# Optimization experiments

Hardware: AMD Instinct MI355X
Metric: run time of the kernel (lower is better)

The kernel has to match this reference:

```python
import jax, jax.numpy as jnp
import numpy as np

B, C, H, W = 8, 128, 64, 64
K = 3
MID = C // 4  # reduction=4


def setup_inputs() -> dict:
    key = jax.random.key(0)
    ks = jax.random.split(key, 8)
    f = lambda k, s, sc=1.0: jax.random.normal(k, s, dtype=jnp.float32) * sc
    return {
        "X2": f(ks[0], (B, C, H, W)),
        "Y2": f(ks[1], (B, C, H, W)),
        "static_w": f(ks[2], (C, 1, K, K), 0.1),        # depthwise conv weight (OIHW, groups=C)
        "w1": f(ks[3], (2 * MID, 2 * C), 0.05),          # context_conv1 1x1
        "w2": f(ks[4], (2 * MID, 2 * MID), 0.05),        # context_conv2 1x1
        "w3": f(ks[5], (C * K * K, 2 * MID), 0.05),      # context_conv3 1x1
        "ws": f(ks[6], (K * K, 2 * C), 0.05),            # spatial_conv 1x1
        "wf": f(ks[7], (C, 2 * C), 0.05),                # fusion_conv 1x1
    }


def _c1x1(w, x):
    # 1x1 conv, no bias: (O,I) x (B,I,H,W) -> (B,O,H,W)
    return jnp.einsum('oc,bchw->bohw', w, x)


def reference(X2, Y2, static_w, w1, w2, w3, ws, wf):
    Bn, Cn, Hn, Wn = X2.shape
    Kn = static_w.shape[-1]
    pad = (Kn - 1) // 2

    # static depthwise conv
    Xs = jax.lax.conv_general_dilated(
        X2, static_w, window_strides=(1, 1), padding='SAME',
        feature_group_count=Cn, dimension_numbers=('NCHW', 'OIHW', 'NCHW'))

    Fc = jnp.concatenate([Xs, Y2], axis=1)  # (B, 2C, H, W)

    # SE-style context branch: 1x1 conv -> global avg pool -> 1x1 -> relu -> 1x1
    ctx = _c1x1(w1, Fc).mean(axis=(2, 3))                  # (B, 2*mid)
    ctx = jax.nn.relu(jnp.einsum('oc,bc->bo', w2, ctx))    # (B, 2*mid)
    channel_filter = jnp.einsum('oc,bc->bo', w3, ctx)      # (B, C*k*k)
    channel_filter = channel_filter.reshape(Bn, Cn, Kn * Kn, 1, 1)

    spatial_filter = _c1x1(ws, Fc).reshape(Bn, 1, Kn * Kn, Hn, Wn)
    dynamic_filter = channel_filter + spatial_filter       # (B, C, k*k, H, W)

    # unfold X2: patch order matches F.unfold (channel-major, kernel row-major)
    Xp = jnp.pad(X2, ((0, 0), (0, 0), (pad, pad), (pad, pad)))
    patches = jnp.stack(
        [Xp[:, :, i:i + Hn, j:j + Wn] for i in range(Kn) for j in range(Kn)],
        axis=2)                                            # (B, C, k*k, H, W)

    dynamic_out = (patches * dynamic_filter).sum(axis=2)   # (B, C, H, W)

    out = _c1x1(wf, jnp.concatenate([Xs, dynamic_out], axis=1))
    return out
```

## Files before the change

kernel.cpp:

```cpp
#include <hip/hip_runtime.h>
#include <hip/hip_bf16.h>

#define Bn 8
#define Cn 128
#define Hn 64
#define Wn 64
#define HWn 4096
#define KK 9

typedef short short8 __attribute__((ext_vector_type(8)));
typedef float f32x4 __attribute__((ext_vector_type(4)));

__device__ inline unsigned short f2b(float v) {
    __hip_bfloat16 h = __float2bfloat16(v);
    return *reinterpret_cast<unsigned short*>(&h);
}

__global__ __launch_bounds__(256) void k_pre(
    const float* __restrict__ X2, const float* __restrict__ Y2,
    float* __restrict__ pws)
{
    int bc = blockIdx.x, t = threadIdx.x;
    const float4* xp = (const float4*)(X2 + (size_t)bc * HWn);
    const float4* yp = (const float4*)(Y2 + (size_t)bc * HWn);
    float v[10];
#pragma unroll
    for (int k = 0; k < 10; k++) v[k] = 0.f;
#pragma unroll
    for (int i = 0; i < 4; i++) {
        int q = t + i * 256;
        float4 x = xp[q], y = yp[q];
        float s4 = x.x + x.y + x.z + x.w;
        v[0] += s4;
        v[5] += y.x + y.y + y.z + y.w;
        int px = q * 4, h = px >> 6, w4 = px & 63;
        if (h == 0)   v[1] += s4;
        if (h == 63)  v[2] += s4;
        if (w4 == 0)  v[3] += x.x;
        if (w4 == 60) v[4] += x.w;
        if (px == 0)    v[6] += x.x;
        if (px == 60)   v[7] += x.w;
        if (px == 4032) v[8] += x.x;
        if (px == 4092) v[9] += x.w;
    }
#pragma unroll
    for (int k = 0; k < 10; k++)
#pragma unroll
        for (int off = 32; off; off >>= 1)
            v[k] += __shfl_down(v[k], off);
    __shared__ float red[4][10];
    int lane = t & 63, wv = t >> 6;
    if (lane == 0) {
#pragma unroll
        for (int k = 0; k < 10; k++) red[wv][k] = v[k];
    }
    __syncthreads();
    if (t < 10) pws[bc * 10 + t] = red[0][t] + red[1][t] + red[2][t] + red[3][t];
}

__global__ __launch_bounds__(256) void k_ctx(
    const float* __restrict__ pws, const float* __restrict__ sw,
    const float* __restrict__ w1, const float* __restrict__ w2,
    const float* __restrict__ w3, const float* __restrict__ wf,
    const float* __restrict__ wsp, float* __restrict__ cf,
    unsigned short* __restrict__ wfb, unsigned short* __restrict__ wsb)
{
    int blk = blockIdx.x, b = blk >> 2, qd = blk & 3;
    int t = threadIdx.x;
    for (int i = t; i < 1024; i += 256) {
        int j = blk * 1024 + i;
        wfb[j] = f2b(wf[j]);
    }
    {
        int j = blk * 128 + t;
        if (t < 128) {
            int tt = j >> 8, c = j & 255;
            wsb[j] = (tt < KK) ? f2b(wsp[tt * 256 + c]) : (unsigned short)0;
        }
    }
    __shared__ float mfc[256], c1[64], c2[64];
    if (t < 128) {
        const float* S = pws + (b * Cn + t) * 10;
        float T = S[0];
        float R[3]  = { S[2], 0.f, S[1] };
        float Cc[3] = { S[4], 0.f, S[3] };
        float Xc[3][3] = {{S[9], 0.f, S[8]}, {0.f, 0.f, 0.f}, {S[7], 0.f, S[6]}};
        float a = 0.f;
#pragma unroll
        for (int i = 0; i < 3; i++)
#pragma unroll
            for (int j = 0; j < 3; j++)
                a += sw[t * 9 + i * 3 + j] * (T - R[i] - Cc[j] + Xc[i][j]);
        mfc[t] = a * (1.f / HWn);
    } else {
        mfc[t] = pws[(b * Cn + (t - 128)) * 10 + 5] * (1.f / HWn);
    }
    __syncthreads();
    if (t < 64) {
        const float4* wr = (const float4*)(w1 + t * 256);
        float a = 0.f;
        for (int c = 0; c < 64; c++) {
            float4 v = wr[c];
            a += v.x * mfc[c*4] + v.y * mfc[c*4+1] + v.z * mfc[c*4+2] + v.w * mfc[c*4+3];
        }
        c1[t] = a;
    }
    __syncthreads();
    if (t < 64) {
        const float4* wr = (const float4*)(w2 + t * 64);
        float a = 0.f;
        for (int c = 0; c < 16; c++) {
            float4 v = wr[c];
            a += v.x * c1[c*4] + v.y * c1[c*4+1] + v.z * c1[c*4+2] + v.w * c1[c*4+3];
        }
        c2[t] = fmaxf(a, 0.f);
    }
    __syncthreads();
    for (int j = qd * 288 + t; j < qd * 288 + 288; j += 256) {
        const float4* wr = (const float4*)(w3 + j * 64);
        float a = 0.f;
        for (int c = 0; c < 16; c++) {
            float4 v = wr[c];
            a += v.x * c2[c*4] + v.y * c2[c*4+1] + v.z * c2[c*4+2] + v.w * c2[c*4+3];
        }
        cf[b * Cn * KK + j] = a;
    }
}

__global__ __launch_bounds__(512, 4) void k_main(
    const float* __restrict__ X2, const float* __restrict__ Y2,
    const float* __restrict__ sw,
    const unsigned short* __restrict__ wfb, const unsigned short* __restrict__ wsb,
    const float* __restrict__ cf, float* __restrict__ out)
{
    __shared__ unsigned short sFt[2][Wn][Cn];
    __shared__ float sSf[KK][Wn];
    __shared__ float sCfP[Cn][12];
    __shared__ float sSwP[Cn][12];

    int bid = blockIdx.x;
    int b = bid & 7, h = bid >> 3;
    int t = threadIdx.x;
    int w = t & 63, cg = t >> 6;
    int swz = (w & 7) << 3;
    int c0 = cg * 16;

    for (int i = t; i < Cn * KK; i += 512) {
        int c = i / 9, q = i - c * 9;
        sSwP[c][q] = sw[i];
        sCfP[c][q] = cf[b * Cn * KK + i];
    }
    __syncthreads();

    const float* xcol = X2 + (size_t)(b * Cn + c0) * HWn + h * Wn + w;
    const float* ycol = Y2 + (size_t)(b * Cn + c0) * HWn + h * Wn + w;
    bool hm = h > 0, hp = h < Hn - 1;
    bool wm = w > 0, wp = w < Wn - 1;

    float tap[16][3];

    {
        unsigned int px[4], py[4];
#pragma unroll
        for (int i = 0; i < 16; i++) {
            int c = c0 + i;
            const float* xp = xcol + (size_t)i * HWn;
            float r0 = hm ? xp[-Wn] : 0.f;
            float r1 = xp[0];
            float r2 = hp ? xp[Wn] : 0.f;
            tap[i][0] = r0; tap[i][1] = r1; tap[i][2] = r2;
            float4 k0 = *(const float4*)&sSwP[c][0];
            float4 k1 = *(const float4*)&sSwP[c][4];
            float  k8 = sSwP[c][8];
            float xl0 = __shfl_up(r0, 1), xr0 = __shfl_down(r0, 1);
            float xl1 = __shfl_up(r1, 1), xr1 = __shfl_down(r1, 1);
            float xl2 = __shfl_up(r2, 1), xr2 = __shfl_down(r2, 1);
            if (!wm) { xl0 = 0.f; xl1 = 0.f; xl2 = 0.f; }
            if (!wp) { xr0 = 0.f; xr1 = 0.f; xr2 = 0.f; }
            float a = k0.x * xl0 + k0.y * r0 + k0.z * xr0
                    + k0.w * xl1 + k1.x * r1 + k1.y * xr1
                    + k1.z * xl2 + k1.w * r2 + k8 * xr2;
            float yv = ycol[(size_t)i * HWn];
            unsigned int ah = f2b(a), yh = f2b(yv);
            int sub = i & 7;
            if ((sub & 1) == 0) { px[sub >> 1] = ah; py[sub >> 1] = yh; }
            else { px[sub >> 1] |= ah << 16; py[sub >> 1] |= yh << 16; }
            if (sub == 7) {
                int col = (c - 7) ^ swz;
                *(uint4*)(&sFt[0][w][col]) = *(uint4*)px;
                *(uint4*)(&sFt[1][w][col]) = *(uint4*)py;
            }
        }
    }
    __syncthreads();

    {
        int lane = t & 63, wv = t >> 6;
        int l16 = lane & 15, half = lane >> 4, kk = half * 8;
        if (wv < 4) {
            int wA = wv * 16 + l16;
            int swzA = (wA & 7) << 3;
            f32x4 acc = (f32x4){0.f, 0.f, 0.f, 0.f};
#pragma unroll
            for (int ks = 0; ks < 8; ks++) {
                short8 av = *(const short8*)(wsb + l16 * 256 + ks * 32 + kk);
                int col = (((ks & 3) * 32 + kk)) ^ swzA;
                short8 bv = *(const short8*)(&sFt[ks >> 2][wA][0] + col);
                acc = __builtin_amdgcn_mfma_f32_16x16x32_bf16(av, bv, acc, 0, 0, 0);
            }
#pragma unroll
            for (int r = 0; r < 4; r++) {
                int tt = half * 4 + r;
                if (tt < KK) sSf[tt][wA] = acc[r];
            }
        }
    }
    __syncthreads();

    {
        float sfw[9];
#pragma unroll
        for (int q = 0; q < 9; q++) sfw[q] = sSf[q][w];
        unsigned int pd[4];
#pragma unroll
        for (int i = 0; i < 16; i++) {
            int c = c0 + i;
            float r0 = tap[i][0], r1 = tap[i][1], r2 = tap[i][2];
            float4 e0 = *(const float4*)&sCfP[c][0];
            float4 e1 = *(const float4*)&sCfP[c][4];
            float  e8 = sCfP[c][8];
            float xl0 = __shfl_up(r0, 1), xr0 = __shfl_down(r0, 1);
            float xl1 = __shfl_up(r1, 1), xr1 = __shfl_down(r1, 1);
            float xl2 = __shfl_up(r2, 1), xr2 = __shfl_down(r2, 1);
            if (!wm) { xl0 = 0.f; xl1 = 0.f; xl2 = 0.f; }
            if (!wp) { xr0 = 0.f; xr1 = 0.f; xr2 = 0.f; }
            float a = (e0.x + sfw[0]) * xl0 + (e0.y + sfw[1]) * r0 + (e0.z + sfw[2]) * xr0
                    + (e0.w + sfw[3]) * xl1 + (e1.x + sfw[4]) * r1 + (e1.y + sfw[5]) * xr1
                    + (e1.z + sfw[6]) * xl2 + (e1.w + sfw[7]) * r2 + (e8 + sfw[8]) * xr2;
            unsigned int ah = f2b(a);
            int sub = i & 7;
            if ((sub & 1) == 0) pd[sub >> 1] = ah;
            else pd[sub >> 1] |= ah << 16;
            if (sub == 7) {
                int col = (c - 7) ^ swz;
                *(uint4*)(&sFt[1][w][col]) = *(uint4*)pd;
            }
        }
    }
    __syncthreads();

    {
        int lane = t & 63, wv = t >> 6;
        int l16 = lane & 15, half = lane >> 4, kk = half * 8;
        int o0 = wv * 16;
        f32x4 acc[4];
#pragma unroll
        for (int n = 0; n < 4; n++) acc[n] = (f32x4){0.f, 0.f, 0.f, 0.f};
#pragma unroll
        for (int ks = 0; ks < 8; ks++) {
            int bufi = ks >> 2;
            int kc = (ks & 3) * 32 + kk;
            short8 av = *(const short8*)(wfb + (o0 + l16) * 256 + ks * 32 + kk);
#pragma unroll
            for (int n = 0; n < 4; n++) {
                int wB = n * 16 + l16;
                int col = kc ^ ((wB & 7) << 3);
                short8 bv = *(const short8*)(&sFt[bufi][wB][0] + col);
                acc[n] = __builtin_amdgcn_mfma_f32_16x16x32_bf16(av, bv, acc[n], 0, 0, 0);
            }
        }
        size_t obase = (size_t)b * Cn * HWn + (size_t)h * Wn;
#pragma unroll
        for (int n = 0; n < 4; n++)
#pragma unroll
            for (int r = 0; r < 4; r++) {
                int o = o0 + half * 4 + r;
                out[obase + (size_t)o * HWn + n * 16 + l16] = acc[n][r];
            }
    }
}

extern "C" void kernel_launch(void* const* d_in, const int* in_sizes, int n_in,
                              void* d_out, int out_size, void* d_ws, size_t ws_size,
                              hipStream_t stream) {
    (void)in_sizes; (void)n_in; (void)out_size; (void)ws_size;
    const float* X2  = (const float*)d_in[0];
    const float* Y2  = (const float*)d_in[1];
    const float* sw  = (const float*)d_in[2];
    const float* w1  = (const float*)d_in[3];
    const float* w2  = (const float*)d_in[4];
    const float* w3  = (const float*)d_in[5];
    const float* wsp = (const float*)d_in[6];
    const float* wf  = (const float*)d_in[7];
    float* out = (float*)d_out;

    float* wsf = (float*)d_ws;
    float* pws = wsf;
    float* cf  = wsf + 10240;
    unsigned short* wfb = (unsigned short*)(wsf + 19456);
    unsigned short* wsb = (unsigned short*)(wsf + 35840);

    hipLaunchKernelGGL(k_pre, dim3(Bn * Cn), dim3(256), 0, stream, X2, Y2, pws);
    hipLaunchKernelGGL(k_ctx, dim3(32), dim3(256), 0, stream,
                       pws, sw, w1, w2, w3, wf, wsp, cf, wfb, wsb);
    hipLaunchKernelGGL(k_main, dim3(Bn * Hn), dim3(512), 0, stream,
                       X2, Y2, sw, wfb, wsb, cf, out);
}
```

Baseline: 60.77 us.

## Split main kernel into spatial-filter and fusion kernels, recomputing static conv

```diff
diff --git a/kernel.cpp b/kernel.cpp
--- a/kernel.cpp
+++ b/kernel.cpp
@@ -127,37 +127,30 @@
     }
 }
 
-__global__ __launch_bounds__(512, 4) void k_main(
+__global__ __launch_bounds__(512, 2) void k_sf(
     const float* __restrict__ X2, const float* __restrict__ Y2,
-    const float* __restrict__ sw,
-    const unsigned short* __restrict__ wfb, const unsigned short* __restrict__ wsb,
-    const float* __restrict__ cf, float* __restrict__ out)
+    const float* __restrict__ sw, const unsigned short* __restrict__ wsb,
+    float* __restrict__ sfB)
 {
     __shared__ unsigned short sFt[2][Wn][Cn];
-    __shared__ float sSf[KK][Wn];
-    __shared__ float sCfP[Cn][12];
     __shared__ float sSwP[Cn][12];
 
     int bid = blockIdx.x;
     int b = bid & 7, h = bid >> 3;
     int t = threadIdx.x;
-    int w = t & 63, cg = t >> 6;
+    int w = t & 63, cg = t >> 6, c0 = cg * 16;
     int swz = (w & 7) << 3;
-    int c0 = cg * 16;
 
     for (int i = t; i < Cn * KK; i += 512) {
         int c = i / 9, q = i - c * 9;
         sSwP[c][q] = sw[i];
-        sCfP[c][q] = cf[b * Cn * KK + i];
-    }
-    __syncthreads();
+    }
 
     const float* xcol = X2 + (size_t)(b * Cn + c0) * HWn + h * Wn + w;
     const float* ycol = Y2 + (size_t)(b * Cn + c0) * HWn + h * Wn + w;
     bool hm = h > 0, hp = h < Hn - 1;
     bool wm = w > 0, wp = w < Wn - 1;
-
-    float tap[16][3];
+    __syncthreads();
 
     {
         unsigned int px[4], py[4];
@@ -168,7 +161,7 @@
             float r0 = hm ? xp[-Wn] : 0.f;
             float r1 = xp[0];
             float r2 = hp ? xp[Wn] : 0.f;
-            tap[i][0] = r0; tap[i][1] = r1; tap[i][2] = r2;
+            float yvv = __builtin_nontemporal_load(ycol + (size_t)i * HWn);
             float4 k0 = *(const float4*)&sSwP[c][0];
             float4 k1 = *(const float4*)&sSwP[c][4];
             float  k8 = sSwP[c][8];
@@ -180,8 +173,7 @@
             float a = k0.x * xl0 + k0.y * r0 + k0.z * xr0
                     + k0.w * xl1 + k1.x * r1 + k1.y * xr1
                     + k1.z * xl2 + k1.w * r2 + k8 * xr2;
-            float yv = ycol[(size_t)i * HWn];
-            unsigned int ah = f2b(a), yh = f2b(yv);
+            unsigned int ah = f2b(a), yh = f2b(yvv);
             int sub = i & 7;
             if ((sub & 1) == 0) { px[sub >> 1] = ah; py[sub >> 1] = yh; }
             else { px[sub >> 1] |= ah << 16; py[sub >> 1] |= yh << 16; }
@@ -194,38 +186,71 @@
     }
     __syncthreads();
 
+    int lane = t & 63, wv = t >> 6;
+    if (wv < 4) {
+        int l16 = lane & 15, half = lane >> 4, kk = half * 8;
+        int wA = wv * 16 + l16;
+        int swzA = (wA & 7) << 3;
+        f32x4 acc = (f32x4){0.f, 0.f, 0.f, 0.f};
+#pragma unroll
+        for (int ks = 0; ks < 8; ks++) {
+            short8 av = *(const short8*)(wsb + l16 * 256 + ks * 32 + kk);
+            int col = (((ks & 3) * 32 + kk)) ^ swzA;
+            short8 bv = *(const short8*)(&sFt[ks >> 2][wA][0] + col);
+            acc = __builtin_amdgcn_mfma_f32_16x16x32_bf16(av, bv, acc, 0, 0, 0);
+        }
+#pragma unroll
+        for (int r = 0; r < 4; r++) {
+            int tt = half * 4 + r;
+            if (tt < KK)
+                sfB[((size_t)b * KK + tt) * HWn + h * Wn + wA] = acc[r];
+        }
+    }
+}
+
+__global__ __launch_bounds__(512, 2) void k_fuse(
+    const float* __restrict__ X2, const float* __restrict__ sw,
+    const float* __restrict__ cf, const float* __restrict__ sfB,
+    const unsigned short* __restrict__ wfb, float* __restrict__ out)
+{
+    __shared__ unsigned short sFt[2][Wn][Cn];
+    __shared__ float sSwP[Cn][12];
+    __shared__ float sCfP[Cn][12];
+
+    int bid = blockIdx.x;
+    int b = bid & 7, h = bid >> 3;
+    int t = threadIdx.x;
+    int w = t & 63, cg = t >> 6, c0 = cg * 16;
+    int swz = (w & 7) << 3;
+
+    for (int i = t; i < Cn * KK; i += 512) {
+        int c = i / 9, q = i - c * 9;
+        sSwP[c][q] = sw[i];
+        sCfP[c][q] = cf[b * Cn * KK + i];
+    }
+
+    float sfw[9];
+#pragma unroll
+    for (int q = 0; q < 9; q++)
+        sfw[q] = sfB[((size_t)b * KK + q) * HWn + h * Wn + w];
+
+    const float* xcol = X2 + (size_t)(b * Cn + c0) * HWn + h * Wn + w;
+    bool hm = h > 0, hp = h < Hn - 1;
+    bool wm = w > 0, wp = w < Wn - 1;
+    __syncthreads();
+
     {
-        int lane = t & 63, wv = t >> 6;
-        int l16 = lane & 15, half = lane >> 4, kk = half * 8;
-        if (wv < 4) {
-            int wA = wv * 16 + l16;
-            int swzA = (wA & 7) << 3;
-            f32x4 acc = (f32x4){0.f, 0.f, 0.f, 0.f};
-#pragma unroll
-            for (int ks = 0; ks < 8; ks++) {
-                short8 av = *(const short8*)(wsb + l16 * 256 + ks * 32 + kk);
-                int col = (((ks & 3) * 32 + kk)) ^ swzA;
-                short8 bv = *(const short8*)(&sFt[ks >> 2][wA][0] + col);
-                acc = __builtin_amdgcn_mfma_f32_16x16x32_bf16(av, bv, acc, 0, 0, 0);
-            }
-#pragma unroll
-            for (int r = 0; r < 4; r++) {
-                int tt = half * 4 + r;
-                if (tt < KK) sSf[tt][wA] = acc[r];
-            }
-        }
-    }
-    __syncthreads();
-
-    {
-        float sfw[9];
-#pragma unroll
-        for (int q = 0; q < 9; q++) sfw[q] = sSf[q][w];
-        unsigned int pd[4];
+        unsigned int px[4], pd[4];
 #pragma unroll
         for (int i = 0; i < 16; i++) {
             int c = c0 + i;
-            float r0 = tap[i][0], r1 = tap[i][1], r2 = tap[i][2];
+            const float* xp = xcol + (size_t)i * HWn;
+            float r0 = hm ? xp[-Wn] : 0.f;
+            float r1 = xp[0];
+            float r2 = hp ? xp[Wn] : 0.f;
+            float4 k0 = *(const float4*)&sSwP[c][0];
+            float4 k1 = *(const float4*)&sSwP[c][4];
+            float  k8 = sSwP[c][8];
             float4 e0 = *(const float4*)&sCfP[c][0];
             float4 e1 = *(const float4*)&sCfP[c][4];
             float  e8 = sCfP[c][8];
@@ -234,15 +259,19 @@
             float xl2 = __shfl_up(r2, 1), xr2 = __shfl_down(r2, 1);
             if (!wm) { xl0 = 0.f; xl1 = 0.f; xl2 = 0.f; }
             if (!wp) { xr0 = 0.f; xr1 = 0.f; xr2 = 0.f; }
-            float a = (e0.x + sfw[0]) * xl0 + (e0.y + sfw[1]) * r0 + (e0.z + sfw[2]) * xr0
+            float a = k0.x * xl0 + k0.y * r0 + k0.z * xr0
+                    + k0.w * xl1 + k1.x * r1 + k1.y * xr1
+                    + k1.z * xl2 + k1.w * r2 + k8 * xr2;
+            float d = (e0.x + sfw[0]) * xl0 + (e0.y + sfw[1]) * r0 + (e0.z + sfw[2]) * xr0
                     + (e0.w + sfw[3]) * xl1 + (e1.x + sfw[4]) * r1 + (e1.y + sfw[5]) * xr1
                     + (e1.z + sfw[6]) * xl2 + (e1.w + sfw[7]) * r2 + (e8 + sfw[8]) * xr2;
-            unsigned int ah = f2b(a);
+            unsigned int ah = f2b(a), dh = f2b(d);
             int sub = i & 7;
-            if ((sub & 1) == 0) pd[sub >> 1] = ah;
-            else pd[sub >> 1] |= ah << 16;
+            if ((sub & 1) == 0) { px[sub >> 1] = ah; pd[sub >> 1] = dh; }
+            else { px[sub >> 1] |= ah << 16; pd[sub >> 1] |= dh << 16; }
             if (sub == 7) {
                 int col = (c - 7) ^ swz;
+                *(uint4*)(&sFt[0][w][col]) = *(uint4*)px;
                 *(uint4*)(&sFt[1][w][col]) = *(uint4*)pd;
             }
         }
@@ -275,7 +304,8 @@
 #pragma unroll
             for (int r = 0; r < 4; r++) {
                 int o = o0 + half * 4 + r;
-                out[obase + (size_t)o * HWn + n * 16 + l16] = acc[n][r];
+                __builtin_nontemporal_store(
+                    acc[n][r], &out[obase + (size_t)o * HWn + n * 16 + l16]);
             }
     }
 }
@@ -299,10 +329,13 @@
     float* cf  = wsf + 10240;
     unsigned short* wfb = (unsigned short*)(wsf + 19456);
     unsigned short* wsb = (unsigned short*)(wsf + 35840);
+    float* sfB = wsf + 37888;
 
     hipLaunchKernelGGL(k_pre, dim3(Bn * Cn), dim3(256), 0, stream, X2, Y2, pws);
     hipLaunchKernelGGL(k_ctx, dim3(32), dim3(256), 0, stream,
                        pws, sw, w1, w2, w3, wf, wsp, cf, wfb, wsb);
-    hipLaunchKernelGGL(k_main, dim3(Bn * Hn), dim3(512), 0, stream,
-                       X2, Y2, sw, wfb, wsb, cf, out);
-}
+    hipLaunchKernelGGL(k_sf, dim3(Bn * Hn), dim3(512), 0, stream,
+                       X2, Y2, sw, wsb, sfB);
+    hipLaunchKernelGGL(k_fuse, dim3(Bn * Hn), dim3(512), 0, stream,
+                       X2, sw, cf, sfB, wfb, out);
+}
```

Result: faster. 56.38 us (-7.2%).
